# Kernel tuning notes

Hardware: AMD Instinct MI355X
Metric: run time of the kernel (lower is better)

Reference implementation:

```python
import jax, jax.numpy as jnp
import numpy as np

BATCH = 2
SEQ = 2048
DIM = 2048
HEADS = 16
DIM_HEAD = 64
DIM_INNER = HEADS * DIM_HEAD  # 1024
SOFTCAP = 50.0
EPS = 1e-12


def setup_inputs() -> dict:
    key = jax.random.key(0)
    k1, k2, k3, k4 = jax.random.split(key, 4)
    x = jax.random.normal(k1, (BATCH, SEQ, DIM), dtype=jnp.float32)
    # RMSNorm gamma param (initialized near zero in the torch module)
    gamma = jax.random.normal(k2, (DIM,), dtype=jnp.float32) * 0.02
    # Linear weights stored already-transposed: x @ W
    w_qkv = jax.random.normal(k3, (DIM, 3 * DIM_INNER), dtype=jnp.float32) * (DIM ** -0.5)
    w_out = jax.random.normal(k4, (DIM_INNER, DIM), dtype=jnp.float32) * (DIM_INNER ** -0.5)
    # (type, offset, length) triples per batch; bidirectional attention inside each span
    modalities = jnp.array(
        [[[0, 256, 256], [0, 1024, 512]],
         [[0, 128, 256], [0, 1536, 384]]], dtype=jnp.int32)
    return dict(x=x, gamma=gamma, w_qkv=w_qkv, w_out=w_out, modalities=modalities)


def _transfusion_attn_mask(seq_len, modalities):
    # causal | (q in span AND kv in span)  -> Bool[b, i, j]
    seq = jnp.arange(seq_len)
    causal = seq[:, None] >= seq[None, :]                      # [i, j]
    offsets = modalities[..., 1]                                # [b, m]
    ends = offsets + modalities[..., 2]                         # [b, m]
    q_in = seq[None, None, :] >= offsets[..., None]             # [b, m, i]
    kv_in = seq[None, None, :] < ends[..., None]                # [b, m, j]
    is_modality = jnp.any(q_in[..., :, None] & kv_in[..., None, :], axis=1)  # [b, i, j]
    return causal[None] | is_modality


def _rmsnorm(x, gamma):
    n = jnp.sqrt(jnp.sum(x * x, axis=-1, keepdims=True))
    x = x / jnp.maximum(n, EPS)
    return x * (DIM ** 0.5) * (gamma + 1.0)


def reference(x, gamma, w_qkv, w_out, modalities):
    xn = _rmsnorm(x, gamma)
    qkv = xn @ w_qkv                                            # [b, n, 3*h*d]
    qkv = qkv.reshape(BATCH, SEQ, 3, HEADS, DIM_HEAD)
    qkv = jnp.transpose(qkv, (2, 0, 3, 1, 4))                   # [3, b, h, n, d]
    q, k, v = qkv[0], qkv[1], qkv[2]
    q = q * (DIM_HEAD ** -0.5)
    sim = jnp.einsum('bhid,bhjd->bhij', q, k)
    sim = jnp.tanh(sim / SOFTCAP) * SOFTCAP                     # softclamp
    mask = _transfusion_attn_mask(SEQ, modalities)              # [b, i, j]
    neg = -jnp.finfo(sim.dtype).max
    sim = jnp.where(mask[:, None, :, :], sim, neg)
    attn = jax.nn.softmax(sim, axis=-1)
    out = jnp.einsum('bhij,bhjd->bhid', attn, v)
    out = jnp.transpose(out, (0, 2, 1, 3)).reshape(BATCH, SEQ, DIM_INNER)
    return out @ w_out
```

## Files before the change

### kernel.cpp

```cpp
#include <hip/hip_runtime.h>
#include <hip/hip_bf16.h>

typedef unsigned short u16;
typedef unsigned int u32;
typedef __attribute__((ext_vector_type(8))) short short8;
typedef __attribute__((ext_vector_type(4))) float f32x4;
typedef __attribute__((ext_vector_type(4))) u16 u16x4;

#define DEV __device__ __forceinline__

DEV u16 f2bf(float f) {
    union { float f; u32 u; } v; v.f = f;
    u32 r = v.u;
    u32 lsb = (r >> 16) & 1u;
    r += 0x7fffu + lsb;
    return (u16)(r >> 16);
}

DEV void gload_lds16(const u16* g, u16* l) {
    __builtin_amdgcn_global_load_lds(
        (const __attribute__((address_space(1))) u32*)(const void*)g,
        (__attribute__((address_space(3))) u32*)(void*)l,
        16, 0, 0);
}

__global__ void prep(const float* __restrict__ x, const float* __restrict__ gamma,
                     const float* __restrict__ w_qkv, const float* __restrict__ w_out,
                     u16* __restrict__ xn, u16* __restrict__ wqkvT, u16* __restrict__ woutT) {
    __shared__ float tile[32][33];
    __shared__ float red[4];
    int id = blockIdx.x;
    int t = threadIdx.x;
    if (id < 8192) {
        const float* in; u16* out; int R, C, bx, by;
        if (id < 6144) { in = w_qkv; out = wqkvT; R = 2048; C = 3072; bx = id % 96; by = id / 96; }
        else { id -= 6144; in = w_out; out = woutT; R = 1024; C = 2048; bx = id % 64; by = id / 64; }
        int tx = t & 31, ty = t >> 5;
        int c0 = bx * 32, r0 = by * 32;
#pragma unroll
        for (int i = 0; i < 4; i++)
            tile[ty * 4 + i][tx] = in[(size_t)(r0 + ty * 4 + i) * C + c0 + tx];
        __syncthreads();
#pragma unroll
        for (int i = 0; i < 4; i++)
            out[(size_t)(c0 + ty * 4 + i) * R + r0 + tx] = f2bf(tile[tx][ty * 4 + i]);
    } else {
        int row = id - 8192;
        const float4* xr = (const float4*)(x + (size_t)row * 2048);
        float4 a = xr[t];
        float4 b = xr[256 + t];
        float ss = a.x * a.x + a.y * a.y + a.z * a.z + a.w * a.w +
                   b.x * b.x + b.y * b.y + b.z * b.z + b.w * b.w;
#pragma unroll
        for (int off = 32; off; off >>= 1) ss += __shfl_xor(ss, off);
        if ((t & 63) == 0) red[t >> 6] = ss;
        __syncthreads();
        float tot = red[0] + red[1] + red[2] + red[3];
        float n = sqrtf(tot);
        float inv = 45.254833995939045f / fmaxf(n, 1e-12f);
        const float4* gr = (const float4*)gamma;
        float4 g0 = gr[t], g1 = gr[256 + t];
        u16x4 o0 = { f2bf(a.x * inv * (g0.x + 1.f)), f2bf(a.y * inv * (g0.y + 1.f)),
                     f2bf(a.z * inv * (g0.z + 1.f)), f2bf(a.w * inv * (g0.w + 1.f)) };
        u16x4 o1 = { f2bf(b.x * inv * (g1.x + 1.f)), f2bf(b.y * inv * (g1.y + 1.f)),
                     f2bf(b.z * inv * (g1.z + 1.f)), f2bf(b.w * inv * (g1.w + 1.f)) };
        u16x4* xo = (u16x4*)(xn + (size_t)row * 2048);
        xo[t] = o0;
        xo[256 + t] = o1;
    }
}

template <int EPI, int BN, int CCOL>
__global__ __launch_bounds__(512, 1) void gemmcf(
    const u16* __restrict__ A, const u16* __restrict__ BT,
    int M, int N, int K,
    float* __restrict__ Cout,
    u16* __restrict__ qb, u16* __restrict__ kb, u16* __restrict__ vT) {
    constexpr int HN = BN / 2;
    constexpr int NF2 = BN / 64;
    constexpr int NG0 = (NF2 + 1) / 2;
    constexpr bool B2 = (HN * 8) > 512;
    __shared__ __align__(16) u16 As[2][2][8192];
    __shared__ __align__(16) u16 Bs[2][2][HN * 64];
    int t = threadIdx.x, lane = t & 63, wid = t >> 6;
    int g = lane >> 4, r = lane & 15;
    int wm = wid >> 2, wn = wid & 3;
    int bhalf = wn >> 1;
    int cb0w = (wn & 1) * (BN / 4);
    int rsw = r & 7;

    int id = blockIdx.x;
    int xcd = id & 7, slot = id >> 3;
    int by = (xcd >> 1) * 4 + slot / CCOL;
    int bx = (xcd & 1) * CCOL + slot % CCOL;
    int brow = by * 256, bcol = bx * BN;

    int gsl = (t & 7) ^ ((t >> 3) & 7);
    const u16* Ag = A + (size_t)(brow + (t >> 3)) * K + gsl * 8;
    const u16* Bg = BT + (size_t)(bcol + (t >> 3)) * K + gsl * 8;
    int dstc = t * 8;

    f32x4 acc[2][4][NF2] = {};
    short8 areg[4][2], breg[NF2][2];
    int NT = K >> 6;

#define STG_A(bf_, kt_, h_) { \
        gload_lds16(Ag + (size_t)((h_) * 128) * K + (kt_) * 64, &As[bf_][h_][dstc]); \
        gload_lds16(Ag + (size_t)((h_) * 128 + 64) * K + (kt_) * 64, &As[bf_][h_][4096 + dstc]); }
#define STG_B(bf_, kt_, h_) { \
        gload_lds16(Bg + (size_t)((h_) * HN) * K + (kt_) * 64, &Bs[bf_][h_][dstc]); \
        if constexpr (B2) { if (t < 256) \
            gload_lds16(Bg + (size_t)((h_) * HN + 64) * K + (kt_) * 64, &Bs[bf_][h_][4096 + dstc]); } }
#define RD_A(qm_) { \
    _Pragma("unroll") for (int mf = 0; mf < 4; mf++) \
    _Pragma("unroll") for (int ks = 0; ks < 2; ks++) \
        areg[mf][ks] = *(const short8*)&As[buf][qm_][(wm * 64 + mf * 16 + r) * 64 + (((ks << 2) + g) ^ rsw) * 8]; }
#define RD_B() { \
    _Pragma("unroll") for (int nf = 0; nf < NF2; nf++) \
    _Pragma("unroll") for (int ks = 0; ks < 2; ks++) \
        breg[nf][ks] = *(const short8*)&Bs[buf][bhalf][(cb0w + nf * 16 + r) * 64 + (((ks << 2) + g) ^ rsw) * 8]; }
#define MFMA_G(qm_, nf0_, nf1_) { \
    __builtin_amdgcn_s_setprio(1); \
    _Pragma("unroll") for (int ks = 0; ks < 2; ks++) \
    _Pragma("unroll") for (int mf = 0; mf < 4; mf++) \
    _Pragma("unroll") for (int nf = nf0_; nf < nf1_; nf++) \
        acc[qm_][mf][nf] = __builtin_amdgcn_mfma_f32_16x16x32_bf16( \
            areg[mf][ks], breg[nf][ks], acc[qm_][mf][nf], 0, 0, 0); \
    __builtin_amdgcn_s_setprio(0); }
#define SCHEDB() __builtin_amdgcn_sched_barrier(0)
#define BAR() __builtin_amdgcn_s_barrier()

    STG_A(0, 0, 0); STG_A(0, 0, 1); STG_B(0, 0, 0); STG_B(0, 0, 1);
    if (NT > 1) { STG_A(1, 1, 0); STG_A(1, 1, 1); }
    if (NT > 1) { asm volatile("s_waitcnt vmcnt(4)" ::: "memory"); }
    else        { asm volatile("s_waitcnt vmcnt(0)" ::: "memory"); }
    SCHEDB();
    BAR();

    for (int kt = 0; kt < NT; ++kt) {
        int buf = kt & 1, ob = buf ^ 1;
        bool s1 = kt + 1 < NT, s2 = kt + 2 < NT;

        RD_B(); RD_A(0);
        if (s1) STG_B(ob, kt + 1, 1);
        asm volatile("s_waitcnt lgkmcnt(0)" ::: "memory");
        SCHEDB();
        MFMA_G(0, 0, NG0);
        BAR();

        if (s1) STG_B(ob, kt + 1, 0);
        if (s2) STG_A(buf, kt + 2, 0);
        MFMA_G(0, NG0, NF2);
        BAR();

        RD_A(1);
        asm volatile("s_waitcnt lgkmcnt(0)" ::: "memory");
        SCHEDB();
        MFMA_G(1, 0, NG0);
        BAR();

        if (s2) STG_A(buf, kt + 2, 1);
        MFMA_G(1, NG0, NF2);
        if (s2)      { asm volatile("s_waitcnt vmcnt(4)" ::: "memory"); }
        else if (s1) { asm volatile("s_waitcnt vmcnt(0)" ::: "memory"); }
        SCHEDB();
        BAR();
    }
#undef STG_A
#undef STG_B
#undef RD_A
#undef RD_B
#undef MFMA_G
#undef SCHEDB
#undef BAR

    if (EPI == 0) {
#pragma unroll
        for (int qm = 0; qm < 2; qm++)
#pragma unroll
            for (int mf = 0; mf < 4; mf++)
#pragma unroll
                for (int nf = 0; nf < NF2; nf++) {
                    int cb = bcol + bhalf * HN + cb0w + nf * 16 + r;
                    int which = cb >> 10;
                    int hd = cb & 1023;
                    int hh = hd >> 6, d = hd & 63;
#pragma unroll
                    for (int j = 0; j < 4; j++) {
                        int rr = brow + qm * 128 + wm * 64 + mf * 16 + 4 * g + j;
                        int b = rr >> 11, nn = rr & 2047;
                        float v = acc[qm][mf][nf][j];
                        size_t bh = (size_t)(b * 16 + hh);
                        if (which == 0)      qb[(bh * 2048 + nn) * 64 + d] = f2bf(v * 0.125f);
                        else if (which == 1) kb[(bh * 2048 + nn) * 64 + d] = f2bf(v);
                        else                 vT[(bh * 64 + d) * 2048 + nn] = f2bf(v);
                    }
                }
    } else {
#pragma unroll
        for (int qm = 0; qm < 2; qm++)
#pragma unroll
            for (int mf = 0; mf < 4; mf++)
#pragma unroll
                for (int nf = 0; nf < NF2; nf++) {
                    int cb = bcol + bhalf * HN + cb0w + nf * 16 + r;
#pragma unroll
                    for (int j = 0; j < 4; j++) {
                        int rr = brow + qm * 128 + wm * 64 + mf * 16 + 4 * g + j;
                        Cout[(size_t)rr * N + cb] = acc[qm][mf][nf][j];
                    }
                }
    }
}

__global__ __launch_bounds__(256, 3) void flash_attn(
    const u16* __restrict__ q, const u16* __restrict__ kk, const u16* __restrict__ vT,
    const int* __restrict__ mods, u16* __restrict__ attn_out) {
    __shared__ __align__(16) u16 Ks[2][4096];
    __shared__ __align__(16) u16 Vs[2][4096];
    __shared__ __align__(16) u16 Plds[4][16][72];
    int t = threadIdx.x, lane = t & 63, wave = t >> 6;
    int g = lane >> 4, r = lane & 15;
    int h = blockIdx.x, b = blockIdx.y;
    int qs = (31 - blockIdx.z) * 64;
    int bh = b * 16 + h;
    int qbase = qs + wave * 16;

    int off0 = mods[b * 6 + 1], end0 = off0 + mods[b * 6 + 2];
    int off1 = mods[b * 6 + 4], end1 = off1 + mods[b * 6 + 5];

    const u16* Qp = q + ((size_t)bh * 2048 + qbase) * 64;
    short8 qf0 = *(const short8*)(Qp + (size_t)r * 64 + 8 * g);
    short8 qf1 = *(const short8*)(Qp + (size_t)r * 64 + 32 + 8 * g);

    int iq = qbase + r;
    int lim0 = (iq >= off0) ? end0 : 0;
    int lim1 = (iq >= off1) ? end1 : 0;
    int rowlim = max(iq + 1, max(lim0, lim1));

    int jlb = qs + 64;
    if (qs + 63 >= off0) jlb = max(jlb, end0);
    if (qs + 63 >= off1) jlb = max(jlb, end1);

    const u16* Kp = kk + (size_t)bh * 2048 * 64;
    const u16* Vp = vT + (size_t)bh * 64 * 2048;
    u16* Pw = &Plds[wave][0][0];

    f32x4 ot[4] = {};
    float psA = 0.f, psB = 0.f;
    int sw = r & 7;

    auto stage64 = [&](const u16* gbase, int gstride, u16* lds) {
#pragma unroll
        for (int i = 0; i < 2; i++) {
            int c = i * 256 + t;
            int row = c >> 3;
            int gsl = (c & 7) ^ (row & 7);
            gload_lds16(gbase + (size_t)row * gstride + 8 * gsl,
                        lds + (size_t)(c & ~63) * 8);
        }
    };

    stage64(Kp, 64, Ks[0]);
    stage64(Vp, 2048, Vs[0]);
    int buf = 0;

    for (int jb = 0; jb < jlb; jb += 64) {
        if (jb + 64 < jlb) {
            stage64(Kp + (size_t)(jb + 64) * 64, 64, Ks[buf ^ 1]);
            stage64(Vp + (jb + 64), 2048, Vs[buf ^ 1]);
            asm volatile("s_waitcnt vmcnt(4)" ::: "memory");
        } else {
            asm volatile("s_waitcnt vmcnt(0)" ::: "memory");
        }
        __builtin_amdgcn_s_barrier();
        const u16* Kt = Ks[buf];
        const u16* Vt = Vs[buf];

        f32x4 st[4];
#pragma unroll
        for (int tt = 0; tt < 4; tt++) {
            int row = 16 * tt + r;
            short8 kf0 = *(const short8*)&Kt[(size_t)(row * 8 + (g ^ sw)) * 8];
            short8 kf1 = *(const short8*)&Kt[(size_t)(row * 8 + ((4 + g) ^ sw)) * 8];
            f32x4 z = {};
            z = __builtin_amdgcn_mfma_f32_16x16x32_bf16(kf0, qf0, z, 0, 0, 0);
            z = __builtin_amdgcn_mfma_f32_16x16x32_bf16(kf1, qf1, z, 0, 0, 0);
            st[tt] = z;
        }
#pragma unroll
        for (int tt = 0; tt < 4; tt++) {
            int kvb = jb + 16 * tt + 4 * g;
            float p0, p1, p2, p3;
#pragma unroll
            for (int j = 0; j < 4; j++) {
                float x = st[tt][j];
                float x2 = x * x;
                float inner = __builtin_fmaf(x2, 2.1333333e-8f, -1.3333333e-4f);
                float poly = __builtin_fmaf(x2, inner, 1.0f);
                float pv = __expf(x * poly);
                pv = (kvb + j < rowlim) ? pv : 0.f;
                if (j == 0) p0 = pv; else if (j == 1) p1 = pv;
                else if (j == 2) p2 = pv; else p3 = pv;
            }
            psA += p0 + p1;
            psB += p2 + p3;
            u32 pk0, pk1;
            asm("v_cvt_pk_bf16_f32 %0, %1, %2" : "=v"(pk0) : "v"(p0), "v"(p1));
            asm("v_cvt_pk_bf16_f32 %0, %1, %2" : "=v"(pk1) : "v"(p2), "v"(p3));
            *(u32*)&Pw[r * 72 + 16 * tt + 4 * g] = pk0;
            *(u32*)&Pw[r * 72 + 16 * tt + 4 * g + 2] = pk1;
        }
        short8 pf0 = *(const short8*)&Pw[r * 72 + 8 * g];
        short8 pf1 = *(const short8*)&Pw[r * 72 + 32 + 8 * g];
#pragma unroll
        for (int dt = 0; dt < 4; dt++) {
            int row = 16 * dt + r;
            short8 vf0 = *(const short8*)&Vt[(size_t)(row * 8 + (g ^ sw)) * 8];
            short8 vf1 = *(const short8*)&Vt[(size_t)(row * 8 + ((4 + g) ^ sw)) * 8];
            ot[dt] = __builtin_amdgcn_mfma_f32_16x16x32_bf16(vf0, pf0, ot[dt], 0, 0, 0);
            ot[dt] = __builtin_amdgcn_mfma_f32_16x16x32_bf16(vf1, pf1, ot[dt], 0, 0, 0);
        }
        asm volatile("s_waitcnt lgkmcnt(0)" ::: "memory");
        __builtin_amdgcn_s_barrier();
        buf ^= 1;
    }

    float lrow = psA + psB;
    lrow += __shfl_xor(lrow, 16);
    lrow += __shfl_xor(lrow, 32);
    float inv = 1.f / lrow;
    u16* Op = attn_out + ((size_t)(b * 2048 + qbase + r)) * 1024 + h * 64;
#pragma unroll
    for (int dt = 0; dt < 4; dt++) {
        u16x4 o = { f2bf(ot[dt][0] * inv), f2bf(ot[dt][1] * inv),
                    f2bf(ot[dt][2] * inv), f2bf(ot[dt][3] * inv) };
        *(u16x4*)(Op + dt * 16 + 4 * g) = o;
    }
}

extern "C" void kernel_launch(void* const* d_in, const int* in_sizes, int n_in,
                              void* d_out, int out_size, void* d_ws, size_t ws_size,
                              hipStream_t stream) {
    const float* x = (const float*)d_in[0];
    const float* gamma = (const float*)d_in[1];
    const float* w_qkv = (const float*)d_in[2];
    const float* w_out = (const float*)d_in[3];
    const int* mods = (const int*)d_in[4];
    float* out = (float*)d_out;

    u16* ws = (u16*)d_ws;
    u16* xn    = ws;
    u16* wqkvT = ws + 8388608;
    u16* woutT = ws + 14680064;
    u16* qb    = ws + 16777216;
    u16* kb    = ws + 20971520;
    u16* vT    = ws + 25165824;
    u16* ao    = ws + 29360128;

    prep<<<dim3(12288), dim3(256), 0, stream>>>(x, gamma, w_qkv, w_out, xn, wqkvT, woutT);
    gemmcf<0, 192, 8><<<dim3(256), dim3(512), 0, stream>>>(xn, wqkvT, 4096, 3072, 2048,
                                                           nullptr, qb, kb, vT);
    flash_attn<<<dim3(16, 2, 32), dim3(256), 0, stream>>>(qb, kb, vT, mods, ao);
    gemmcf<1, 128, 8><<<dim3(256), dim3(512), 0, stream>>>(ao, woutT, 4096, 2048, 1024,
                                                           out, nullptr, nullptr, nullptr);
}
```

Baseline: 164.1 us.

## Replace QKV GEMM with smaller-tile triple-buffered kernel allowing multiple blocks per CU

Adds a new GEMM kernel for the QKV projection that uses 128x192 tiles with K-step 32 and a three-stage LDS ring buffer, with launch bounds that allow up to four blocks per CU. Its grid is 512 blocks, each mapped to a tile through an XCD-aware swizzle. The aim is better occupancy and latency hiding than the previous one-block-per-CU kernel with large tiles. In exchange, each tile is smaller, so there is less operand reuse per block and more barriers per unit of K.

```diff
diff --git a/kernel.cpp b/kernel.cpp
--- a/kernel.cpp
+++ b/kernel.cpp
@@ -67,6 +67,121 @@
         u16x4* xo = (u16x4*)(xn + (size_t)row * 2048);
         xo[t] = o0;
         xo[256 + t] = o1;
+    }
+}
+
+template <int EPI, int BN>
+__global__ __launch_bounds__(512, 4) void gemmw(
+    const u16* __restrict__ A, const u16* __restrict__ BT,
+    int M, int N, int K,
+    float* __restrict__ Cout,
+    u16* __restrict__ qb, u16* __restrict__ kb, u16* __restrict__ vT) {
+    constexpr int NF = BN / 64;
+    constexpr bool BX = (BN * 4) > 512;
+    __shared__ __align__(16) u16 As[3][4096];
+    __shared__ __align__(16) u16 Bs[3][BN * 32];
+    int t = threadIdx.x, lane = t & 63, wid = t >> 6;
+    int g = lane >> 4, r = lane & 15;
+    int wm = wid >> 2, wn = wid & 3;
+    int csw = (r >> 1) & 3;
+
+    int id = blockIdx.x;
+    int xcd = id & 7, slot = id >> 3;
+    int by = (xcd >> 1) * 8 + (slot >> 3);
+    int bx = (xcd & 1) * 8 + (slot & 7);
+    int brow = by * 128, bcol = bx * BN;
+
+    int gk = (t & 3) ^ ((t >> 3) & 3);
+    const u16* Ag = A + (size_t)(brow + (t >> 2)) * K + gk * 8;
+    const u16* Bg = BT + (size_t)(bcol + (t >> 2)) * K + gk * 8;
+    const u16* Bg2 = BT + (size_t)(bcol + 128 + (t >> 2)) * K + gk * 8;
+    int dst = (t & ~63) * 8;
+
+    f32x4 acc[4][NF] = {};
+    short8 areg[4], breg[NF];
+    int NT = K >> 5;
+
+#define STG(kt_, b3_) { \
+        gload_lds16(Ag + (kt_) * 32, &As[b3_][dst]); \
+        gload_lds16(Bg + (kt_) * 32, &Bs[b3_][dst]); \
+        if constexpr (BX) { if (t < 256) gload_lds16(Bg2 + (kt_) * 32, &Bs[b3_][4096 + dst]); } }
+#define SCHEDB() __builtin_amdgcn_sched_barrier(0)
+#define BAR() __builtin_amdgcn_s_barrier()
+
+    STG(0, 0);
+    if (NT > 1) STG(1, 1);
+    asm volatile("s_waitcnt vmcnt(0)" ::: "memory");
+    SCHEDB();
+    BAR();
+
+    int c0 = 0;
+    for (int kt = 0; kt < NT; ++kt) {
+        int c2 = c0 + 2; if (c2 >= 3) c2 -= 3;
+        bool s1 = kt + 1 < NT, s2 = kt + 2 < NT;
+        if (s2) STG(kt + 2, c2);
+        const u16* Ac = As[c0];
+        const u16* Bc = Bs[c0];
+#pragma unroll
+        for (int mf = 0; mf < 4; mf++)
+            areg[mf] = *(const short8*)&Ac[(wm * 64 + mf * 16 + r) * 32 + (g ^ csw) * 8];
+#pragma unroll
+        for (int nf = 0; nf < NF; nf++)
+            breg[nf] = *(const short8*)&Bc[(wn * (BN / 4) + nf * 16 + r) * 32 + (g ^ csw) * 8];
+        asm volatile("s_waitcnt lgkmcnt(0)" ::: "memory");
+        SCHEDB();
+        __builtin_amdgcn_s_setprio(1);
+#pragma unroll
+        for (int mf = 0; mf < 4; mf++)
+#pragma unroll
+            for (int nf = 0; nf < NF; nf++)
+                acc[mf][nf] = __builtin_amdgcn_mfma_f32_16x16x32_bf16(areg[mf], breg[nf], acc[mf][nf], 0, 0, 0);
+        __builtin_amdgcn_s_setprio(0);
+        if (s2) {
+            if (BX && wid < 4) { asm volatile("s_waitcnt vmcnt(3)" ::: "memory"); }
+            else               { asm volatile("s_waitcnt vmcnt(2)" ::: "memory"); }
+        } else if (s1) {
+            asm volatile("s_waitcnt vmcnt(0)" ::: "memory");
+        }
+        SCHEDB();
+        BAR();
+        c0 = (c0 + 1 == 3) ? 0 : c0 + 1;
+    }
+#undef STG
+#undef SCHEDB
+#undef BAR
+
+    if (EPI == 0) {
+#pragma unroll
+        for (int mf = 0; mf < 4; mf++)
+#pragma unroll
+            for (int nf = 0; nf < NF; nf++) {
+                int cb = bcol + wn * (BN / 4) + nf * 16 + r;
+                int which = cb >> 10;
+                int hd = cb & 1023;
+                int hh = hd >> 6, d = hd & 63;
+#pragma unroll
+                for (int j = 0; j < 4; j++) {
+                    int rr = brow + wm * 64 + mf * 16 + 4 * g + j;
+                    int b = rr >> 11, nn = rr & 2047;
+                    float v = acc[mf][nf][j];
+                    size_t bh = (size_t)(b * 16 + hh);
+                    if (which == 0)      qb[(bh * 2048 + nn) * 64 + d] = f2bf(v * 0.125f);
+                    else if (which == 1) kb[(bh * 2048 + nn) * 64 + d] = f2bf(v);
+                    else                 vT[(bh * 64 + d) * 2048 + nn] = f2bf(v);
+                }
+            }
+    } else {
+#pragma unroll
+        for (int mf = 0; mf < 4; mf++)
+#pragma unroll
+            for (int nf = 0; nf < NF; nf++) {
+                int cb = bcol + wn * (BN / 4) + nf * 16 + r;
+#pragma unroll
+                for (int j = 0; j < 4; j++) {
+                    int rr = brow + wm * 64 + mf * 16 + 4 * g + j;
+                    Cout[(size_t)rr * N + cb] = acc[mf][nf][j];
+                }
+            }
     }
 }
 
@@ -359,8 +474,8 @@
     u16* ao    = ws + 29360128;
 
     prep<<<dim3(12288), dim3(256), 0, stream>>>(x, gamma, w_qkv, w_out, xn, wqkvT, woutT);
-    gemmcf<0, 192, 8><<<dim3(256), dim3(512), 0, stream>>>(xn, wqkvT, 4096, 3072, 2048,
-                                                           nullptr, qb, kb, vT);
+    gemmw<0, 192><<<dim3(512), dim3(512), 0, stream>>>(xn, wqkvT, 4096, 3072, 2048,
+                                                       nullptr, qb, kb, vT);
     flash_attn<<<dim3(16, 2, 32), dim3(256), 0, stream>>>(qb, kb, vT, mods, ao);
     gemmcf<1, 128, 8><<<dim3(256), dim3(512), 0, stream>>>(ao, woutT, 4096, 2048, 1024,
                                                            out, nullptr, nullptr, nullptr);
```

Measured after the change: 166.2 us. Within noise of the previous version (+1.3%).
